# Performance work log

Hardware: AMD Instinct MI355X
Metric: run time of the kernel (lower is better)

## Reference

```python
import jax, jax.numpy as jnp
import numpy as np

N_HEADS = 32
N_KV_HEADS = 8
HEAD_DIM = 128
N_REP = N_HEADS // N_KV_HEADS


def apply_rope(x, cos, sin):
    # x: [B, S, H, D]; cos/sin: [S_max, D//2]
    S = x.shape[1]
    c = cos[:S][None, :, None, :]
    s = sin[:S][None, :, None, :]
    x_even = x[..., ::2]
    x_odd = x[..., 1::2]
    out = jnp.stack([x_even * c - x_odd * s, x_even * s + x_odd * c], axis=-1)
    return out.reshape(x.shape)


def setup_inputs() -> dict:
    key = jax.random.key(0)
    ks = jax.random.split(key, 8)
    B, S, D = 2, 2048, 4096
    x = jax.random.normal(ks[0], (B, S, D), dtype=jnp.float32)
    # RoPE tables
    pos = jnp.arange(S, dtype=jnp.float32)[:, None]
    inv_freq = 1.0 / (10000.0 ** (jnp.arange(0, HEAD_DIM, 2, dtype=jnp.float32) / HEAD_DIM))
    ang = pos * inv_freq[None, :]  # [S, HEAD_DIM//2]
    cos = jnp.cos(ang)
    sin = jnp.sin(ang)
    # causal additive mask [1,1,S,S]
    tril = jnp.tril(jnp.ones((S, S), dtype=bool))
    mask = jnp.where(tril, 0.0, -1e9).astype(jnp.float32)[None, None]
    sc = 0.02
    Wq = jax.random.normal(ks[1], (D, N_HEADS * HEAD_DIM), dtype=jnp.float32) * sc
    Wk = jax.random.normal(ks[2], (D, N_KV_HEADS * HEAD_DIM), dtype=jnp.float32) * sc
    Wv = jax.random.normal(ks[3], (D, N_KV_HEADS * HEAD_DIM), dtype=jnp.float32) * sc
    Wo = jax.random.normal(ks[4], (N_HEADS * HEAD_DIM, D), dtype=jnp.float32) * sc
    return {"x": x, "cos": cos, "sin": sin, "mask": mask,
            "Wq": Wq, "Wk": Wk, "Wv": Wv, "Wo": Wo}


def reference(x, cos, sin, mask, Wq, Wk, Wv, Wo):
    B, S, D = x.shape
    q = (x @ Wq).reshape(B, S, N_HEADS, HEAD_DIM)
    k = (x @ Wk).reshape(B, S, N_KV_HEADS, HEAD_DIM)
    v = (x @ Wv).reshape(B, S, N_KV_HEADS, HEAD_DIM)
    q = apply_rope(q, cos, sin)
    k = apply_rope(k, cos, sin)
    # repeat_interleave KV heads to match query heads
    k = jnp.repeat(k, N_REP, axis=2)
    v = jnp.repeat(v, N_REP, axis=2)
    q = q.transpose(0, 2, 1, 3)  # [B, H, S, D]
    k = k.transpose(0, 2, 1, 3)
    v = v.transpose(0, 2, 1, 3)
    scale = HEAD_DIM ** -0.5
    scores = jnp.einsum('bhqd,bhkd->bhqk', q, k) * scale + mask
    attn = jax.nn.softmax(scores, axis=-1)
    out = jnp.einsum('bhqk,bhkd->bhqd', attn, v)
    out = out.transpose(0, 2, 1, 3).reshape(B, S, N_HEADS * HEAD_DIM)
    return out @ Wo
```

## Files before the change

### kernel.cpp

```cpp
#include <hip/hip_runtime.h>

typedef __attribute__((ext_vector_type(8))) short short8;
typedef __attribute__((ext_vector_type(4))) float f32x4;
typedef __attribute__((ext_vector_type(16))) float f32x16;
typedef __attribute__((ext_vector_type(4))) unsigned short u16x4;
typedef __attribute__((ext_vector_type(8))) unsigned short u16x8;

typedef __attribute__((address_space(3))) void lds_void;
typedef __attribute__((address_space(1))) void g_void;

#define GL16(g, l) __builtin_amdgcn_global_load_lds((g_void*)(g), (lds_void*)(l), 16, 0, 0)
#define EXP2F(x) __builtin_exp2f(x)

__device__ inline float b2f(unsigned short u) {
  union { unsigned u; float f; } v; v.u = ((unsigned)u) << 16; return v.f;
}
__device__ inline unsigned short f2b(float f) {
  union { float f; unsigned u; } v; v.f = f;
  unsigned r = v.u + 0x7FFFu + ((v.u >> 16) & 1u);
  return (unsigned short)(r >> 16);
}
__device__ inline unsigned short f2b_rne(float f) {
  unsigned u;
  asm("v_cvt_pk_bf16_f32 %0, %1, %2" : "=v"(u) : "v"(f), "v"(f));
  return (unsigned short)u;
}
__device__ inline unsigned short cvtb(float v) { return f2b(v); }
__device__ inline unsigned short cvtb(unsigned short v) { return v; }

__global__ __launch_bounds__(256) void conv_f32_bf16(const float* __restrict__ in,
                                                     unsigned short* __restrict__ out, long n) {
  long i = ((long)blockIdx.x * 256 + threadIdx.x) * 4;
  if (i >= n) return;
  f32x4 v = *(const f32x4*)(in + i);
  u16x4 o;
  o[0] = f2b(v[0]); o[1] = f2b(v[1]); o[2] = f2b(v[2]); o[3] = f2b(v[3]);
  *(u16x4*)(out + i) = o;
}

template <typename TIN>
__global__ __launch_bounds__(256) void transpose_bf16(const TIN* __restrict__ in,
                                                      unsigned short* __restrict__ out,
                                                      int R, int C, int ldin) {
  __shared__ unsigned short tile[32][33];
  int c0 = blockIdx.x * 32, r0 = blockIdx.y * 32;
  int tx = threadIdx.x & 31, ty = threadIdx.x >> 5;
#pragma unroll
  for (int i = ty; i < 32; i += 8)
    tile[i][tx] = cvtb(in[(long)(r0 + i) * ldin + c0 + tx]);
  __syncthreads();
#pragma unroll
  for (int i = ty; i < 32; i += 8)
    out[(long)(c0 + i) * R + r0 + tx] = tile[tx][i];
}

template <int MODE>
__global__ __launch_bounds__(256, 3) void gemm_m97(const unsigned short* __restrict__ A,
                                                   const unsigned short* __restrict__ Bt,
                                                   void* __restrict__ C,
                                                   const float* __restrict__ cosp,
                                                   const float* __restrict__ sinp,
                                                   int M, int N, int K) {
  __shared__ unsigned short As[128 * 64];
  __shared__ unsigned short Bs[128 * 64];
  const int tid = threadIdx.x;
  const int lane = tid & 63;
  const int wid = tid >> 6;
  const int wr = wid >> 1, wc = wid & 1;
  const int l31 = lane & 31, lh = lane >> 5;
  const int xr = l31 & 7;
  const int nbn = N >> 7;
  const int bm = blockIdx.x / nbn, bn = blockIdx.x % nbn;

  const long K2 = (long)K * 2;
  const int csw = ((tid & 7) ^ ((tid >> 3) & 7)) << 4;
  const char* gA = (const char*)A + ((long)bm * 128 + (tid >> 3)) * K2 + csw;
  const char* gB = (const char*)Bt + ((long)bn * 128 + (tid >> 3)) * K2 + csw;
  char* dA = (char*)As + tid * 16;
  char* dB = (char*)Bs + tid * 16;

  f32x16 acc[2][2];
#pragma unroll
  for (int m = 0; m < 2; m++)
#pragma unroll
    for (int n = 0; n < 2; n++)
#pragma unroll
      for (int i = 0; i < 16; i++) acc[m][n][i] = 0.f;

  const int offA0 = (wr * 64 + l31) * 128;
  const int offB0 = (wc * 64 + l31) * 128;

  const int NT = K >> 6;
  for (int t = 0; t < NT; ++t) {
    __syncthreads();
    const long ko = (long)t * 128;
    GL16(gA + ko, dA);
    GL16(gA + ko + 32 * K2, dA + 4096);
    GL16(gA + ko + 64 * K2, dA + 8192);
    GL16(gA + ko + 96 * K2, dA + 12288);
    GL16(gB + ko, dB);
    GL16(gB + ko + 32 * K2, dB + 4096);
    GL16(gB + ko + 64 * K2, dB + 8192);
    GL16(gB + ko + 96 * K2, dB + 12288);
    __syncthreads();
#pragma unroll
    for (int kk = 0; kk < 4; kk++) {
      const int co = (((kk * 2 + lh) ^ xr) << 4);
      short8 a0 = *(const short8*)((const char*)As + offA0 + co);
      short8 a1 = *(const short8*)((const char*)As + offA0 + 4096 + co);
      short8 b0 = *(const short8*)((const char*)Bs + offB0 + co);
      short8 b1 = *(const short8*)((const char*)Bs + offB0 + 4096 + co);
      acc[0][0] = __builtin_amdgcn_mfma_f32_32x32x16_bf16(a0, b0, acc[0][0], 0, 0, 0);
      acc[0][1] = __builtin_amdgcn_mfma_f32_32x32x16_bf16(a0, b1, acc[0][1], 0, 0, 0);
      acc[1][0] = __builtin_amdgcn_mfma_f32_32x32x16_bf16(a1, b0, acc[1][0], 0, 0, 0);
      acc[1][1] = __builtin_amdgcn_mfma_f32_32x32x16_bf16(a1, b1, acc[1][1], 0, 0, 0);
    }
  }

  const long crow0 = (long)bm * 128 + wr * 64 + 4 * lh;
  const int ccol0 = bn * 128 + wc * 64 + l31;
  const float qscale = 0.08838834764831845f * 1.44269504088896341f;
#pragma unroll
  for (int m = 0; m < 2; m++)
#pragma unroll
    for (int n = 0; n < 2; n++)
#pragma unroll
      for (int reg = 0; reg < 16; reg++) {
        long row = crow0 + m * 32 + (reg & 3) + 8 * (reg >> 2);
        int col = ccol0 + n * 32;
        float v = acc[m][n][reg];
        if (MODE == 0) {
          ((float*)C)[row * N + col] = v;
        } else {
          float other = __shfl_xor(v, 1, 64);
          float out = v;
          if (col < 5120) {
            int s = (int)(row & 2047);
            int ib = (col & 127) >> 1;
            float cc = cosp[s * 64 + ib], ss = sinp[s * 64 + ib];
            out = (col & 1) ? (other * ss + v * cc) : (v * cc - other * ss);
            if (col < 4096) out *= qscale;
          }
          ((unsigned short*)C)[row * N + col] = f2b_rne(out);
        }
      }
}

__global__ __launch_bounds__(256) void attn_kernel(const unsigned short* __restrict__ QKV,
                                                   const unsigned short* __restrict__ Vt,
                                                   unsigned short* __restrict__ O,
                                                   int S, int BS) {
  __shared__ unsigned short Ks[64 * 128];
  __shared__ unsigned short Vs[128 * 64];
  __shared__ unsigned short Ps[4][16 * 68];
  const int tid = threadIdx.x, wave = tid >> 6, lane = tid & 63;
  const int lrow = lane & 15, kgrp = lane >> 4;
  const int nqt = S >> 6, nqt2 = nqt >> 1;
  int bid = blockIdx.x;
  const int qp = bid % nqt2; bid /= nqt2;
  const int h = bid & 31;
  const int b = bid >> 5;
  const int kh = h >> 2;
  const long rowbase = (long)b * S;

  const char* kg = (const char*)(QKV + rowbase * 6144 + 4096 + kh * 128)
                   + (tid >> 4) * 12288 + (((tid & 15) ^ ((tid >> 4) & 7)) * 16);
  const char* vg = (const char*)(Vt + (long)(kh * 128 + (tid >> 3)) * BS + rowbase)
                   + (((tid & 7) ^ ((tid >> 3) & 7)) * 16);
  char* lK = (char*)Ks + wave * 1024;
  char* lV = (char*)Vs + wave * 1024;

  for (int pass = 0; pass < 2; pass++) {
    const int qt = pass ? (nqt - 1 - qp) : qp;
    const int qbase = qt * 64;
    const int q0 = qbase + wave * 16;

    short8 qf[4];
    {
      const unsigned short* qpt = QKV + (rowbase + q0 + lrow) * 6144 + h * 128 + kgrp * 8;
#pragma unroll
      for (int dc = 0; dc < 4; dc++) qf[dc] = *(const short8*)(qpt + dc * 32);
    }
    f32x4 oacc[8];
#pragma unroll
    for (int dt = 0; dt < 8; dt++) oacc[dt] = (f32x4){0.f, 0.f, 0.f, 0.f};
    float mrun[4] = {-1e30f, -1e30f, -1e30f, -1e30f};
    float lrun[4] = {0.f, 0.f, 0.f, 0.f};

    const int kv_end = qbase + 64;
    for (int kv0 = 0; kv0 < kv_end; kv0 += 64) {
      __syncthreads();
#pragma unroll
      for (int p = 0; p < 4; p++)
        GL16(kg + (long)(kv0 + p * 16) * 12288, lK + p * 4096);
#pragma unroll
      for (int p = 0; p < 4; p++)
        GL16(vg + (long)kv0 * 2 + (long)p * 32 * BS * 2, lV + p * 4096);
      __syncthreads();

      f32x4 sc[4];
#pragma unroll
      for (int n = 0; n < 4; n++) {
        f32x4 s = (f32x4){0.f, 0.f, 0.f, 0.f};
#pragma unroll
        for (int dc = 0; dc < 4; dc++) {
          short8 kf = *(const short8*)(Ks + (n * 16 + lrow) * 128 + (((dc * 4 + kgrp) ^ (lrow & 7)) << 3));
          s = __builtin_amdgcn_mfma_f32_16x16x32_bf16(qf[dc], kf, s, 0, 0, 0);
        }
        sc[n] = s;
      }

      if (kv0 + 63 > q0) {
#pragma unroll
        for (int r = 0; r < 4; r++) {
          const int qg = q0 + kgrp * 4 + r;
#pragma unroll
          for (int n = 0; n < 4; n++) {
            int kgi = kv0 + n * 16 + lrow;
            if (kgi > qg) sc[n][r] = -1e30f;
          }
        }
      }

      float mx[4];
#pragma unroll
      for (int r = 0; r < 4; r++) {
        float m0 = fmaxf(fmaxf(sc[0][r], sc[1][r]), fmaxf(sc[2][r], sc[3][r]));
#pragma unroll
        for (int d = 1; d < 16; d <<= 1) m0 = fmaxf(m0, __shfl_xor(m0, d, 64));
        mx[r] = m0;
      }
      bool grow = false;
#pragma unroll
      for (int r = 0; r < 4; r++) grow = grow || (mx[r] > mrun[r] + 8.f);

      if (__all(!grow)) {
#pragma unroll
        for (int r = 0; r < 4; r++) {
          float psum = 0.f;
#pragma unroll
          for (int n = 0; n < 4; n++) {
            float pv = EXP2F(sc[n][r] - mrun[r]);
            psum += pv;
            Ps[wave][(kgrp * 4 + r) * 68 + n * 16 + lrow] = f2b_rne(pv);
          }
          lrun[r] += psum;
        }
      } else {
#pragma unroll
        for (int r = 0; r < 4; r++) {
          float mnew = fmaxf(mrun[r], mx[r]);
          float corr = EXP2F(mrun[r] - mnew);
          mrun[r] = mnew;
          float psum = 0.f;
#pragma unroll
          for (int n = 0; n < 4; n++) {
            float pv = EXP2F(sc[n][r] - mnew);
            psum += pv;
            Ps[wave][(kgrp * 4 + r) * 68 + n * 16 + lrow] = f2b_rne(pv);
          }
          lrun[r] = lrun[r] * corr + psum;
#pragma unroll
          for (int dt = 0; dt < 8; dt++) oacc[dt][r] *= corr;
        }
      }
      asm volatile("s_waitcnt lgkmcnt(0)" ::: "memory");
#pragma unroll
      for (int kc = 0; kc < 2; kc++) {
        short8 pa = *(const short8*)(&Ps[wave][lrow * 68 + kc * 32 + kgrp * 8]);
#pragma unroll
        for (int dt = 0; dt < 8; dt++) {
          short8 vb = *(const short8*)(Vs + (dt * 16 + lrow) * 64 + (((kc * 4 + kgrp) ^ (lrow & 7)) << 3));
          oacc[dt] = __builtin_amdgcn_mfma_f32_16x16x32_bf16(pa, vb, oacc[dt], 0, 0, 0);
        }
      }
    }

    float inv[4];
#pragma unroll
    for (int r = 0; r < 4; r++) {
      float l = lrun[r];
#pragma unroll
      for (int d = 1; d < 16; d <<= 1) l += __shfl_xor(l, d, 64);
      inv[r] = 1.f / l;
    }
    unsigned short* op = O + (rowbase + q0 + kgrp * 4) * 4096 + h * 128 + lrow;
#pragma unroll
    for (int dt = 0; dt < 8; dt++)
#pragma unroll
      for (int r = 0; r < 4; r++)
        op[(long)r * 4096 + dt * 16] = f2b_rne(oacc[dt][r] * inv[r]);
  }
}

extern "C" void kernel_launch(void* const* d_in, const int* in_sizes, int n_in,
                              void* d_out, int out_size, void* d_ws, size_t ws_size,
                              hipStream_t stream) {
  const float* x = (const float*)d_in[0];
  const float* cosp = (const float*)d_in[1];
  const float* sinp = (const float*)d_in[2];
  const float* Wq = (const float*)d_in[4];
  const float* Wk = (const float*)d_in[5];
  const float* Wv = (const float*)d_in[6];
  const float* Wo = (const float*)d_in[7];
  const int S = 2048;
  const long M = 4096;

  if (ws_size < 176160768ULL) return;

  char* ws = (char*)d_ws;
  unsigned short* xb   = (unsigned short*)(ws);
  unsigned short* Wqt  = (unsigned short*)(ws + 33554432);
  unsigned short* Wkt  = (unsigned short*)(ws + 67108864);
  unsigned short* Wvt  = (unsigned short*)(ws + 75497472);
  unsigned short* Wot  = (unsigned short*)(ws + 83886080);
  unsigned short* QKVb = (unsigned short*)(ws + 117440512);
  unsigned short* Vtg  = (unsigned short*)(ws + 167772160);
  unsigned short* AO   = xb;

  conv_f32_bf16<<<16384, 256, 0, stream>>>(x, xb, M * 4096);
  transpose_bf16<float><<<dim3(128, 128), 256, 0, stream>>>(Wq, Wqt, 4096, 4096, 4096);
  transpose_bf16<float><<<dim3(32, 128), 256, 0, stream>>>(Wk, Wkt, 4096, 1024, 1024);
  transpose_bf16<float><<<dim3(32, 128), 256, 0, stream>>>(Wv, Wvt, 4096, 1024, 1024);
  transpose_bf16<float><<<dim3(128, 128), 256, 0, stream>>>(Wo, Wot, 4096, 4096, 4096);

  gemm_m97<2><<<1536, 256, 0, stream>>>(xb, Wqt, QKVb, cosp, sinp, 4096, 6144, 4096);
  transpose_bf16<unsigned short><<<dim3(32, 128), 256, 0, stream>>>(QKVb + 5120, Vtg, 4096, 1024, 6144);

  attn_kernel<<<1024, 256, 0, stream>>>(QKVb, Vtg, AO, S, 4096);

  gemm_m97<0><<<1024, 256, 0, stream>>>(AO, Wot, d_out, nullptr, nullptr, 4096, 4096, 4096);
}
```

Before: 659.4 us.

## Merge weight transposes into one launch, swizzle P tile, raise occupancy bounds

```diff
diff --git a/kernel.cpp b/kernel.cpp
--- a/kernel.cpp
+++ b/kernel.cpp
@@ -25,8 +25,6 @@
   asm("v_cvt_pk_bf16_f32 %0, %1, %2" : "=v"(u) : "v"(f), "v"(f));
   return (unsigned short)u;
 }
-__device__ inline unsigned short cvtb(float v) { return f2b(v); }
-__device__ inline unsigned short cvtb(unsigned short v) { return v; }
 
 __global__ __launch_bounds__(256) void conv_f32_bf16(const float* __restrict__ in,
                                                      unsigned short* __restrict__ out, long n) {
@@ -38,29 +36,53 @@
   *(u16x4*)(out + i) = o;
 }
 
-template <typename TIN>
-__global__ __launch_bounds__(256) void transpose_bf16(const TIN* __restrict__ in,
-                                                      unsigned short* __restrict__ out,
-                                                      int R, int C, int ldin) {
+__global__ __launch_bounds__(256) void prep_weights(const float* __restrict__ Wq,
+                                                    const float* __restrict__ Wk,
+                                                    const float* __restrict__ Wv,
+                                                    const float* __restrict__ Wo,
+                                                    unsigned short* __restrict__ Wqkv,
+                                                    unsigned short* __restrict__ Wot) {
+  __shared__ unsigned short tile[32][33];
+  int id = blockIdx.x;
+  const float* src; unsigned short* dst; int C;
+  if (id < 16384)      { src = Wq; dst = Wqkv;            C = 4096; }
+  else if (id < 20480) { src = Wk; dst = Wqkv + 16777216; C = 1024; id -= 16384; }
+  else if (id < 24576) { src = Wv; dst = Wqkv + 20971520; C = 1024; id -= 20480; }
+  else                 { src = Wo; dst = Wot;             C = 4096; id -= 24576; }
+  const int nbx = C >> 5;
+  const int c0 = (id % nbx) * 32, r0 = (id / nbx) * 32;
+  const int tx = threadIdx.x & 31, ty = threadIdx.x >> 5;
+#pragma unroll
+  for (int i = ty; i < 32; i += 8)
+    tile[i][tx] = f2b(src[(long)(r0 + i) * C + c0 + tx]);
+  __syncthreads();
+#pragma unroll
+  for (int i = ty; i < 32; i += 8)
+    dst[(long)(c0 + i) * 4096 + r0 + tx] = tile[tx][i];
+}
+
+__global__ __launch_bounds__(256) void transpose_u16(const unsigned short* __restrict__ in,
+                                                     unsigned short* __restrict__ out,
+                                                     int R, int C, int ldin) {
   __shared__ unsigned short tile[32][33];
   int c0 = blockIdx.x * 32, r0 = blockIdx.y * 32;
   int tx = threadIdx.x & 31, ty = threadIdx.x >> 5;
 #pragma unroll
   for (int i = ty; i < 32; i += 8)
-    tile[i][tx] = cvtb(in[(long)(r0 + i) * ldin + c0 + tx]);
+    tile[i][tx] = in[(long)(r0 + i) * ldin + c0 + tx];
   __syncthreads();
 #pragma unroll
   for (int i = ty; i < 32; i += 8)
     out[(long)(c0 + i) * R + r0 + tx] = tile[tx][i];
 }
 
-template <int MODE>
-__global__ __launch_bounds__(256, 3) void gemm_m97(const unsigned short* __restrict__ A,
-                                                   const unsigned short* __restrict__ Bt,
-                                                   void* __restrict__ C,
-                                                   const float* __restrict__ cosp,
-                                                   const float* __restrict__ sinp,
-                                                   int M, int N, int K) {
+template <int MODE, int MINB>
+__global__ __launch_bounds__(256, MINB) void gemm_m97(const unsigned short* __restrict__ A,
+                                                      const unsigned short* __restrict__ Bt,
+                                                      void* __restrict__ C,
+                                                      const float* __restrict__ cosp,
+                                                      const float* __restrict__ sinp,
+                                                      int M, int N, int K) {
   __shared__ unsigned short As[128 * 64];
   __shared__ unsigned short Bs[128 * 64];
   const int tid = threadIdx.x;
@@ -146,13 +168,13 @@
       }
 }
 
-__global__ __launch_bounds__(256) void attn_kernel(const unsigned short* __restrict__ QKV,
-                                                   const unsigned short* __restrict__ Vt,
-                                                   unsigned short* __restrict__ O,
-                                                   int S, int BS) {
+__global__ __launch_bounds__(256, 4) void attn_kernel(const unsigned short* __restrict__ QKV,
+                                                      const unsigned short* __restrict__ Vt,
+                                                      unsigned short* __restrict__ O,
+                                                      int S, int BS) {
   __shared__ unsigned short Ks[64 * 128];
   __shared__ unsigned short Vs[128 * 64];
-  __shared__ unsigned short Ps[4][16 * 68];
+  __shared__ unsigned short Ps[4][16 * 64];
   const int tid = threadIdx.x, wave = tid >> 6, lane = tid & 63;
   const int lrow = lane & 15, kgrp = lane >> 4;
   const int nqt = S >> 6, nqt2 = nqt >> 1;
@@ -237,18 +259,23 @@
       if (__all(!grow)) {
 #pragma unroll
         for (int r = 0; r < 4; r++) {
+          const int q = kgrp * 4 + r;
+          const int pbase = q * 64;
           float psum = 0.f;
 #pragma unroll
           for (int n = 0; n < 4; n++) {
             float pv = EXP2F(sc[n][r] - mrun[r]);
             psum += pv;
-            Ps[wave][(kgrp * 4 + r) * 68 + n * 16 + lrow] = f2b_rne(pv);
+            int k = n * 16 + lrow;
+            Ps[wave][pbase + ((((k >> 3) ^ (q & 7)) << 3) | (k & 7))] = f2b_rne(pv);
           }
           lrun[r] += psum;
         }
       } else {
 #pragma unroll
         for (int r = 0; r < 4; r++) {
+          const int q = kgrp * 4 + r;
+          const int pbase = q * 64;
           float mnew = fmaxf(mrun[r], mx[r]);
           float corr = EXP2F(mrun[r] - mnew);
           mrun[r] = mnew;
@@ -257,7 +284,8 @@
           for (int n = 0; n < 4; n++) {
             float pv = EXP2F(sc[n][r] - mnew);
             psum += pv;
-            Ps[wave][(kgrp * 4 + r) * 68 + n * 16 + lrow] = f2b_rne(pv);
+            int k = n * 16 + lrow;
+            Ps[wave][pbase + ((((k >> 3) ^ (q & 7)) << 3) | (k & 7))] = f2b_rne(pv);
           }
           lrun[r] = lrun[r] * corr + psum;
 #pragma unroll
@@ -267,7 +295,7 @@
       asm volatile("s_waitcnt lgkmcnt(0)" ::: "memory");
 #pragma unroll
       for (int kc = 0; kc < 2; kc++) {
-        short8 pa = *(const short8*)(&Ps[wave][lrow * 68 + kc * 32 + kgrp * 8]);
+        short8 pa = *(const short8*)(&Ps[wave][lrow * 64 + (((kc * 4 + kgrp) ^ (lrow & 7)) << 3)]);
 #pragma unroll
         for (int dt = 0; dt < 8; dt++) {
           short8 vb = *(const short8*)(Vs + (dt * 16 + lrow) * 64 + (((kc * 4 + kgrp) ^ (lrow & 7)) << 3));
@@ -311,23 +339,18 @@
   char* ws = (char*)d_ws;
   unsigned short* xb   = (unsigned short*)(ws);
   unsigned short* Wqt  = (unsigned short*)(ws + 33554432);
-  unsigned short* Wkt  = (unsigned short*)(ws + 67108864);
-  unsigned short* Wvt  = (unsigned short*)(ws + 75497472);
   unsigned short* Wot  = (unsigned short*)(ws + 83886080);
   unsigned short* QKVb = (unsigned short*)(ws + 117440512);
   unsigned short* Vtg  = (unsigned short*)(ws + 167772160);
   unsigned short* AO   = xb;
 
   conv_f32_bf16<<<16384, 256, 0, stream>>>(x, xb, M * 4096);
-  transpose_bf16<float><<<dim3(128, 128), 256, 0, stream>>>(Wq, Wqt, 4096, 4096, 4096);
-  transpose_bf16<float><<<dim3(32, 128), 256, 0, stream>>>(Wk, Wkt, 4096, 1024, 1024);
-  transpose_bf16<float><<<dim3(32, 128), 256, 0, stream>>>(Wv, Wvt, 4096, 1024, 1024);
-  transpose_bf16<float><<<dim3(128, 128), 256, 0, stream>>>(Wo, Wot, 4096, 4096, 4096);
-
-  gemm_m97<2><<<1536, 256, 0, stream>>>(xb, Wqt, QKVb, cosp, sinp, 4096, 6144, 4096);
-  transpose_bf16<unsigned short><<<dim3(32, 128), 256, 0, stream>>>(QKVb + 5120, Vtg, 4096, 1024, 6144);
+  prep_weights<<<40960, 256, 0, stream>>>(Wq, Wk, Wv, Wo, Wqt, Wot);
+
+  gemm_m97<2, 3><<<1536, 256, 0, stream>>>(xb, Wqt, QKVb, cosp, sinp, 4096, 6144, 4096);
+  transpose_u16<<<dim3(32, 128), 256, 0, stream>>>(QKVb + 5120, Vtg, 4096, 1024, 6144);
 
   attn_kernel<<<1024, 256, 0, stream>>>(QKVb, Vtg, AO, S, 4096);
 
-  gemm_m97<0><<<1024, 256, 0, stream>>>(AO, Wot, d_out, nullptr, nullptr, 4096, 4096, 4096);
-}
+  gemm_m97<0, 4><<<1024, 256, 0, stream>>>(AO, Wot, d_out, nullptr, nullptr, 4096, 4096, 4096);
+}
```

Measured after the change: 792.5 us. 1.2x slower.
